# Performance work log

Measured on AMD Instinct MI355X. Metric: run time of the kernel, lower is better.

The kernel has to match this reference:

```python
import jax, jax.numpy as jnp
import numpy as np

STRIDES = (2, 2, 2)  # from init_kwargs


def _sparse_conv3d_transpose(images, kernel, default_value, base_plane, strides):
    """Sparse masked 3D transposed conv driven by a per-pixel depth base plane.

    images:     [B, Hi, Wi, Di, C]  stored slab of active voxels per pixel
    kernel:     [kH, kW, kD, F, C]
    base_plane: [B, Ho, Wo, 1] int  starting VIRTUAL depth of the output slab
    Output virtual depth of voxel (ho, wo, do) is base_plane[ho, wo] + do.
    Input slab start (in input-depth units) at input pixel (hi, wi) is
    base_plane[hi*sH, wi*sW] // sD. SAME-style padding ((k-1)//2).
    Out-of-slab / out-of-bounds taps read default_value (frozen zero).
    """
    B, Hi, Wi, Di, C = images.shape
    k0, k1, k2, F, _ = kernel.shape
    s0, s1, s2 = strides
    bp = base_plane[..., 0]                       # [B, Ho, Wo]
    Ho, Wo = bp.shape[1], bp.shape[2]
    Do = Di * s2
    p0, p1, p2 = (k0 - 1) // 2, (k1 - 1) // 2, (k2 - 1) // 2
    bp_in = bp[:, ::s0, ::s1] // s2               # [B, Hi, Wi] input slab start
    b_idx = jnp.arange(B)[:, None, None]
    vd = bp[..., None] + jnp.arange(Do)           # [B, Ho, Wo, Do] virtual out depth
    ho = jnp.arange(Ho)
    wo = jnp.arange(Wo)
    out = jnp.zeros((B, Ho, Wo, Do, F), images.dtype)
    for kh in range(k0):
        hn = ho + p0 - kh
        hok = (hn % s0 == 0) & (hn >= 0) & (hn < Hi * s0)
        hi = jnp.clip(hn // s0, 0, Hi - 1)
        for kw in range(k1):
            wn = wo + p1 - kw
            wok = (wn % s1 == 0) & (wn >= 0) & (wn < Wi * s1)
            wi = jnp.clip(wn // s1, 0, Wi - 1)
            sp_ok = hok[None, :, None] & wok[None, None, :]              # [1,Ho,Wo]
            bpg = bp_in[b_idx, hi[None, :, None], wi[None, None, :]]     # [B,Ho,Wo]
            for kd in range(k2):
                dn = vd + p2 - kd                                        # [B,Ho,Wo,Do]
                dok = (dn % s2) == 0
                di = dn // s2 - bpg[..., None]
                mask = sp_ok[..., None] & dok & (di >= 0) & (di < Di)
                dic = jnp.clip(di, 0, Di - 1)
                # gather [B,Ho,Wo,Do,C]
                vals = images[b_idx[..., None], hi[None, :, None, None],
                              wi[None, None, :, None], dic]
                vals = jnp.where(mask[..., None], vals, default_value)
                out = out + jnp.einsum('bhwdc,fc->bhwdf', vals, kernel[kh, kw, kd])
    return out


def setup_inputs() -> dict:
    key = jax.random.key(0)
    k1, k2, k3 = jax.random.split(key, 3)
    B, Hi, Wi, Di, C, F = 2, 64, 64, 32, 16, 8
    images = jax.random.normal(k1, (B, Hi, Wi, Di, C), dtype=jnp.float32)
    base_plane = jax.random.randint(k2, (B, Hi * 2, Wi * 2, 1), 0, 16, dtype=jnp.int32)
    kernel = jax.random.normal(k3, (3, 3, 3, F, C), dtype=jnp.float32) * 0.1
    default_value = jnp.zeros((), dtype=jnp.float32)  # frozen, zeros initializer
    return {"images": images, "base_plane": base_plane,
            "kernel": kernel, "default_value": default_value}


def reference(images, base_plane, kernel, default_value):
    return _sparse_conv3d_transpose(images, kernel, default_value, base_plane, STRIDES)
```

## Files before the change

### kernel.cpp

```cpp
#include <hip/hip_runtime.h>

constexpr int Bc  = 2;
constexpr int HiC = 64, WiC = 64, DiC = 32;
constexpr int Cc  = 16, Fc  = 8;
constexpr int HoC = 128, WoC = 128, DoC = 64;
constexpr int IMG_ELEMS = Bc * HiC * WiC * DiC * Cc;

constexpr int SLAB_SHORTS = DiC * Cc;
constexpr int NSLAB       = 18;
constexpr int ZOFF        = NSLAB * SLAB_SHORTS * 2;

typedef __attribute__((ext_vector_type(8))) short short8;
typedef __attribute__((ext_vector_type(4))) float f32x4;

__device__ alignas(16) const float FZERO[8] = {0, 0, 0, 0, 0, 0, 0, 0};

__device__ __forceinline__ unsigned pk2(float x, float y) {
    unsigned ux = __float_as_uint(x), uy = __float_as_uint(y);
    ux += ((ux >> 16) & 1u) + 0x7FFFu;
    uy += ((uy >> 16) & 1u) + 0x7FFFu;
    return (ux >> 16) | (uy & 0xFFFF0000u);
}
__device__ __forceinline__ short8 pack8(float4 a, float4 b) {
    union { unsigned u[4]; short8 s; } r;
    r.u[0] = pk2(a.x, a.y); r.u[1] = pk2(a.z, a.w);
    r.u[2] = pk2(b.x, b.y); r.u[3] = pk2(b.z, b.w);
    return r.s;
}

__device__ __forceinline__ void gload_lds16(const short* g, short* l) {
    __builtin_amdgcn_global_load_lds(
        (const __attribute__((address_space(1))) void*)(unsigned long long)(const void*)g,
        (__attribute__((address_space(3))) void*)(unsigned long long)(void*)l,
        16, 0, 0);
}

__global__ __launch_bounds__(256)
void imgcvt(const float4* __restrict__ in, uint2* __restrict__ outv, int n4) {
    int i = blockIdx.x * 256 + threadIdx.x;
    if (i < n4) {
        float4 v = in[i];
        uint2 o; o.x = pk2(v.x, v.y); o.y = pk2(v.z, v.w);
        outv[i] = o;
    } else if (i < n4 + 8) {
        uint2 z; z.x = 0u; z.y = 0u;
        outv[i] = z;
    }
}

template<int CLS, int CVT>
__device__ __forceinline__ void doCols(const short* __restrict__ slabs,
                                       const float* __restrict__ img32,
                                       const int*   __restrict__ bp,
                                       const float* __restrict__ kern,
                                       float*       __restrict__ out,
                                       float*       __restrict__ ldsw,
                                       int b, int ho, int wo0, int wi0, int lane) {
    constexpr int NP = (CLS == 0) ? 1 : ((CLS == 3) ? 4 : 2);
    constexpr int OP = (NP + 1) / 2;
    constexpr int KH[4][4] = {{1,0,0,0},{1,1,0,0},{0,2,0,0},{0,0,2,2}};
    constexpr int KW[4][4] = {{1,0,0,0},{0,2,0,0},{1,1,0,0},{0,2,0,2}};

    const int quad = lane >> 4, n = lane & 15;
    const int half = quad >> 1, chalf = quad & 1;
    const int chalfB = chalf * 16;

    short8 bE[NP], bO[OP];
    #pragma unroll
    for (int p = 0; p < NP; ++p) {
        const int kp = KH[CLS][p] * 3 + KW[CLS][p];
        const float* wp = (n < Fc)
            ? kern + (kp * 3 + 2 * half) * 128 + n * 16 + chalf * 8 : FZERO;
        bE[p] = pack8(*(const float4*)wp, *(const float4*)(wp + 4));
    }
    #pragma unroll
    for (int pp = 0; pp < OP; ++pp) {
        const int  PA   = (2 * pp < NP) ? 2 * pp : 0;
        const bool hasB = (2 * pp + 1) < NP;
        const int  PB   = hasB ? (2 * pp + 1) : 0;
        const int kpa = KH[CLS][PA] * 3 + KW[CLS][PA];
        const int kpb = KH[CLS][PB] * 3 + KW[CLS][PB];
        const int kp  = half ? kpb : kpa;
        const bool v  = (n < Fc) && (!half || hasB);
        const float* wp = v ? kern + (kp * 3 + 1) * 128 + n * 16 + chalf * 8 : FZERO;
        bO[pp] = pack8(*(const float4*)wp, *(const float4*)(wp + 4));
    }

    int colx[4], bpcol[4], bpgr[4][NP], pxo[4][NP]; bool pvs[4][NP];
    #pragma unroll
    for (int cc = 0; cc < 4; ++cc) {
        const int wo = wo0 + 2 * cc;
        colx[cc]  = __builtin_amdgcn_readfirstlane((b * HoC + ho) * WoC + wo);
        bpcol[cc] = bp[colx[cc]];
        #pragma unroll
        for (int p = 0; p < NP; ++p) {
            const int kh = KH[CLS][p], kw = KW[CLS][p];
            int hi = (ho + 1 - kh) >> 1; hi = hi > HiC - 1 ? HiC - 1 : hi;
            int wi = (wo + 1 - kw) >> 1; wi = wi > WiC - 1 ? WiC - 1 : wi;
            pvs[cc][p] = (kh != 0 || ho + 1 < HoC) && (kw != 0 || wo + 1 < WoC);
            const int sidx =
                __builtin_amdgcn_readfirstlane((b * HoC + 2 * hi) * WoC + 2 * wi);
            bpgr[cc][p] = bp[sidx];
            if constexpr (CVT) {
                pxo[cc][p] = __builtin_amdgcn_readfirstlane(
                                 ((b * HiC + hi) * WiC + wi) * (DiC * Cc));
            } else {
                const int hidx = (kh == 0) ? 1 : 0;
                pxo[cc][p] = __builtin_amdgcn_readfirstlane(
                                 (hidx * 9 + (wi - wi0)) << 10);
            }
        }
    }

    #pragma unroll
    for (int cc = 0; cc < 4; ++cc) {
        const int bp_col = bpcol[cc];
        const int q      = (bp_col + 1) & 1;
        const int baseE  = (bp_col + q + 1) >> 1;
        const int baseO  = (bp_col + 1 - q) >> 1;
        int sE[NP], sO[NP];
        #pragma unroll
        for (int p = 0; p < NP; ++p) {
            const int bpg = bpgr[cc][p] >> 1;
            sE[p] = pvs[cc][p] ? baseE - bpg : -100000;
            sO[p] = pvs[cc][p] ? baseO - bpg : -100000;
        }

        f32x4 accE[2] = {{0.f,0.f,0.f,0.f},{0.f,0.f,0.f,0.f}};
        f32x4 accO[2] = {{0.f,0.f,0.f,0.f},{0.f,0.f,0.f,0.f}};

        #pragma unroll
        for (int g = 0; g < 2; ++g) {
            #pragma unroll
            for (int p = 0; p < NP; ++p) {
                const int  di = sE[p] + 16 * g + n - half;
                const bool ok = (unsigned)di < (unsigned)DiC;
                short8 a;
                if constexpr (CVT) {
                    const float* ap = ok ? img32 + pxo[cc][p] + di * Cc + chalf * 8 : FZERO;
                    a = pack8(*(const float4*)ap, *(const float4*)(ap + 4));
                } else {
                    const int off = ok ? pxo[cc][p] + di * 32 + chalfB : ZOFF;
                    a = *(const short8*)((const char*)slabs + off);
                }
                accE[g] = __builtin_amdgcn_mfma_f32_16x16x32_bf16(a, bE[p], accE[g], 0, 0, 0);
            }
            #pragma unroll
            for (int pp = 0; pp < OP; ++pp) {
                const int  PA   = (2 * pp < NP) ? 2 * pp : 0;
                const bool hasB = (2 * pp + 1) < NP;
                const int  PB   = hasB ? (2 * pp + 1) : 0;
                const int  sOs  = half ? (hasB ? sO[PB] : -100000) : sO[PA];
                const int  pxs  = half ? pxo[cc][PB] : pxo[cc][PA];
                const int  di = sOs + 16 * g + n;
                const bool ok = (unsigned)di < (unsigned)DiC;
                short8 a;
                if constexpr (CVT) {
                    const float* ap = ok ? img32 + pxs + di * Cc + chalf * 8 : FZERO;
                    a = pack8(*(const float4*)ap, *(const float4*)(ap + 4));
                } else {
                    const int off = ok ? pxs + di * 32 + chalfB : ZOFF;
                    a = *(const short8*)((const char*)slabs + off);
                }
                accO[g] = __builtin_amdgcn_mfma_f32_16x16x32_bf16(a, bO[pp], accO[g], 0, 0, 0);
            }
        }

        __builtin_amdgcn_wave_barrier();
        if (n < Fc) {
            #pragma unroll
            for (int g = 0; g < 2; ++g) {
                #pragma unroll
                for (int r = 0; r < 4; ++r) {
                    const int m2 = 16 * g + quad * 4 + r;
                    ldsw[(2 * m2 + q) * Fc + n]     = accE[g][r];
                    ldsw[(2 * m2 + 1 - q) * Fc + n] = accO[g][r];
                }
            }
        }
        __builtin_amdgcn_wave_barrier();
        float* outc = out + (size_t)colx[cc] * (DoC * Fc);
        *(float4*)(outc + lane * 8)     = *(const float4*)(ldsw + lane * 8);
        *(float4*)(outc + lane * 8 + 4) = *(const float4*)(ldsw + lane * 8 + 4);
        __builtin_amdgcn_wave_barrier();
    }
}

template<int CVT>
__global__ __launch_bounds__(256, 3)
void sconv_mfma(const short* __restrict__ img16, const float* __restrict__ img32,
                const int* __restrict__ bp, const float* __restrict__ kern,
                float* __restrict__ out) {
    __shared__ short slabs[NSLAB * SLAB_SHORTS + 8];
    __shared__ float lds[4 * DoC * Fc];
    const int t = threadIdx.x, wv = t >> 6, lane = t & 63;
    const int b = blockIdx.z, ho = blockIdx.y;
    const int wo0 = (blockIdx.x << 4) + (wv & 1) + ((wv >> 1) << 3);
    const int wi0 = blockIdx.x << 3;
    float* ldsw = lds + wv * (DoC * Fc);

    if constexpr (!CVT) {
        const int nSlab = (ho & 1) ? 18 : 9;
        const int hi0 = ho >> 1;
        int hi1 = (ho + 1) >> 1; if (hi1 > HiC - 1) hi1 = HiC - 1;
        for (int s = wv; s < nSlab; s += 4) {
            const int hi = (s >= 9) ? hi1 : hi0;
            int wi = wi0 + ((s >= 9) ? s - 9 : s); if (wi > WiC - 1) wi = WiC - 1;
            const short* g = img16 + (((b * HiC + hi) * WiC + wi) << 9) + lane * 8;
            gload_lds16(g, &slabs[s << 9]);
        }
        if (t < 8) slabs[NSLAB * SLAB_SHORTS + t] = 0;
        __syncthreads();
    }

    if (ho & 1) {
        if (wv & 1) doCols<3, CVT>(slabs, img32, bp, kern, out, ldsw, b, ho, wo0, wi0, lane);
        else        doCols<2, CVT>(slabs, img32, bp, kern, out, ldsw, b, ho, wo0, wi0, lane);
    } else {
        if (wv & 1) doCols<1, CVT>(slabs, img32, bp, kern, out, ldsw, b, ho, wo0, wi0, lane);
        else        doCols<0, CVT>(slabs, img32, bp, kern, out, ldsw, b, ho, wo0, wi0, lane);
    }
}

extern "C" void kernel_launch(void* const* d_in, const int* in_sizes, int n_in,
                              void* d_out, int out_size, void* d_ws, size_t ws_size,
                              hipStream_t stream) {
    const float* images = (const float*)d_in[0];
    const int*   bp     = (const int*)d_in[1];
    const float* kern   = (const float*)d_in[2];
    float* out = (float*)d_out;

    const size_t needWs = ((size_t)IMG_ELEMS + 32) * sizeof(short);

    dim3 grid(WoC / 16, HoC, Bc), block(256);
    if (ws_size >= needWs) {
        const int n4 = IMG_ELEMS / 4;
        hipLaunchKernelGGL(imgcvt, dim3(n4 / 256 + 1), dim3(256), 0, stream,
                           (const float4*)images, (uint2*)d_ws, n4);
        hipLaunchKernelGGL((sconv_mfma<0>), grid, block, 0, stream,
                           (const short*)d_ws, images, bp, kern, out);
    } else {
        hipLaunchKernelGGL((sconv_mfma<1>), grid, block, 0, stream,
                           (const short*)nullptr, images, bp, kern, out);
    }
}
```

Baseline: 98.62 us.

## Fuse fp32-to-bf16 image conversion into slab staging and drop separate convert kernel

Removes the standalone imgcvt kernel and its bf16 workspace copy. Each block now loads fp32 image slabs directly from global memory, packs them to bf16 in registers, and writes them into LDS before the MFMA loop. This saves one kernel launch and a full read/write pass over the image. In exchange, each block reads twice as many bytes per slab, does the packing arithmetic redundantly across the blocks that share slabs, and gives up the async global_load_lds path.

Measured after the change: 97.50 us. No clear change (-1.1%).

```diff
diff --git a/kernel.cpp b/kernel.cpp
--- a/kernel.cpp
+++ b/kernel.cpp
@@ -4,7 +4,6 @@
 constexpr int HiC = 64, WiC = 64, DiC = 32;
 constexpr int Cc  = 16, Fc  = 8;
 constexpr int HoC = 128, WoC = 128, DoC = 64;
-constexpr int IMG_ELEMS = Bc * HiC * WiC * DiC * Cc;
 
 constexpr int SLAB_SHORTS = DiC * Cc;
 constexpr int NSLAB       = 18;
@@ -28,29 +27,8 @@
     return r.s;
 }
 
-__device__ __forceinline__ void gload_lds16(const short* g, short* l) {
-    __builtin_amdgcn_global_load_lds(
-        (const __attribute__((address_space(1))) void*)(unsigned long long)(const void*)g,
-        (__attribute__((address_space(3))) void*)(unsigned long long)(void*)l,
-        16, 0, 0);
-}
-
-__global__ __launch_bounds__(256)
-void imgcvt(const float4* __restrict__ in, uint2* __restrict__ outv, int n4) {
-    int i = blockIdx.x * 256 + threadIdx.x;
-    if (i < n4) {
-        float4 v = in[i];
-        uint2 o; o.x = pk2(v.x, v.y); o.y = pk2(v.z, v.w);
-        outv[i] = o;
-    } else if (i < n4 + 8) {
-        uint2 z; z.x = 0u; z.y = 0u;
-        outv[i] = z;
-    }
-}
-
-template<int CLS, int CVT>
+template<int CLS>
 __device__ __forceinline__ void doCols(const short* __restrict__ slabs,
-                                       const float* __restrict__ img32,
                                        const int*   __restrict__ bp,
                                        const float* __restrict__ kern,
                                        float*       __restrict__ out,
@@ -101,14 +79,9 @@
             const int sidx =
                 __builtin_amdgcn_readfirstlane((b * HoC + 2 * hi) * WoC + 2 * wi);
             bpgr[cc][p] = bp[sidx];
-            if constexpr (CVT) {
-                pxo[cc][p] = __builtin_amdgcn_readfirstlane(
-                                 ((b * HiC + hi) * WiC + wi) * (DiC * Cc));
-            } else {
-                const int hidx = (kh == 0) ? 1 : 0;
-                pxo[cc][p] = __builtin_amdgcn_readfirstlane(
-                                 (hidx * 9 + (wi - wi0)) << 10);
-            }
+            const int hidx = (kh == 0) ? 1 : 0;
+            pxo[cc][p] = __builtin_amdgcn_readfirstlane(
+                             (hidx * 9 + (wi - wi0)) << 10);
         }
     }
 
@@ -135,14 +108,8 @@
             for (int p = 0; p < NP; ++p) {
                 const int  di = sE[p] + 16 * g + n - half;
                 const bool ok = (unsigned)di < (unsigned)DiC;
-                short8 a;
-                if constexpr (CVT) {
-                    const float* ap = ok ? img32 + pxo[cc][p] + di * Cc + chalf * 8 : FZERO;
-                    a = pack8(*(const float4*)ap, *(const float4*)(ap + 4));
-                } else {
-                    const int off = ok ? pxo[cc][p] + di * 32 + chalfB : ZOFF;
-                    a = *(const short8*)((const char*)slabs + off);
-                }
+                const int  off = ok ? pxo[cc][p] + di * 32 + chalfB : ZOFF;
+                short8 a = *(const short8*)((const char*)slabs + off);
                 accE[g] = __builtin_amdgcn_mfma_f32_16x16x32_bf16(a, bE[p], accE[g], 0, 0, 0);
             }
             #pragma unroll
@@ -154,14 +121,8 @@
                 const int  pxs  = half ? pxo[cc][PB] : pxo[cc][PA];
                 const int  di = sOs + 16 * g + n;
                 const bool ok = (unsigned)di < (unsigned)DiC;
-                short8 a;
-                if constexpr (CVT) {
-                    const float* ap = ok ? img32 + pxs + di * Cc + chalf * 8 : FZERO;
-                    a = pack8(*(const float4*)ap, *(const float4*)(ap + 4));
-                } else {
-                    const int off = ok ? pxs + di * 32 + chalfB : ZOFF;
-                    a = *(const short8*)((const char*)slabs + off);
-                }
+                const int  off = ok ? pxs + di * 32 + chalfB : ZOFF;
+                short8 a = *(const short8*)((const char*)slabs + off);
                 accO[g] = __builtin_amdgcn_mfma_f32_16x16x32_bf16(a, bO[pp], accO[g], 0, 0, 0);
             }
         }
@@ -186,11 +147,9 @@
     }
 }
 
-template<int CVT>
 __global__ __launch_bounds__(256, 3)
-void sconv_mfma(const short* __restrict__ img16, const float* __restrict__ img32,
-                const int* __restrict__ bp, const float* __restrict__ kern,
-                float* __restrict__ out) {
+void sconv_mfma(const float* __restrict__ img, const int* __restrict__ bp,
+                const float* __restrict__ kern, float* __restrict__ out) {
     __shared__ short slabs[NSLAB * SLAB_SHORTS + 8];
     __shared__ float lds[4 * DoC * Fc];
     const int t = threadIdx.x, wv = t >> 6, lane = t & 63;
@@ -199,26 +158,30 @@
     const int wi0 = blockIdx.x << 3;
     float* ldsw = lds + wv * (DoC * Fc);
 
-    if constexpr (!CVT) {
-        const int nSlab = (ho & 1) ? 18 : 9;
-        const int hi0 = ho >> 1;
-        int hi1 = (ho + 1) >> 1; if (hi1 > HiC - 1) hi1 = HiC - 1;
-        for (int s = wv; s < nSlab; s += 4) {
+    const int nSlab = (ho & 1) ? 18 : 9;
+    const int hi0 = ho >> 1;
+    int hi1 = (ho + 1) >> 1; if (hi1 > HiC - 1) hi1 = HiC - 1;
+    #pragma unroll
+    for (int k = 0; k < 5; ++k) {
+        const int s = wv + 4 * k;
+        if (s < nSlab) {
             const int hi = (s >= 9) ? hi1 : hi0;
             int wi = wi0 + ((s >= 9) ? s - 9 : s); if (wi > WiC - 1) wi = WiC - 1;
-            const short* g = img16 + (((b * HiC + hi) * WiC + wi) << 9) + lane * 8;
-            gload_lds16(g, &slabs[s << 9]);
-        }
-        if (t < 8) slabs[NSLAB * SLAB_SHORTS + t] = 0;
-        __syncthreads();
-    }
+            const float* g = img + (((b * HiC + hi) * WiC + wi) << 9) + lane * 8;
+            float4 v0 = *(const float4*)g;
+            float4 v1 = *(const float4*)(g + 4);
+            *(short8*)&slabs[(s << 9) + lane * 8] = pack8(v0, v1);
+        }
+    }
+    if (t < 8) slabs[NSLAB * SLAB_SHORTS + t] = 0;
+    __syncthreads();
 
     if (ho & 1) {
-        if (wv & 1) doCols<3, CVT>(slabs, img32, bp, kern, out, ldsw, b, ho, wo0, wi0, lane);
-        else        doCols<2, CVT>(slabs, img32, bp, kern, out, ldsw, b, ho, wo0, wi0, lane);
+        if (wv & 1) doCols<3>(slabs, bp, kern, out, ldsw, b, ho, wo0, wi0, lane);
+        else        doCols<2>(slabs, bp, kern, out, ldsw, b, ho, wo0, wi0, lane);
     } else {
-        if (wv & 1) doCols<1, CVT>(slabs, img32, bp, kern, out, ldsw, b, ho, wo0, wi0, lane);
-        else        doCols<0, CVT>(slabs, img32, bp, kern, out, ldsw, b, ho, wo0, wi0, lane);
+        if (wv & 1) doCols<1>(slabs, bp, kern, out, ldsw, b, ho, wo0, wi0, lane);
+        else        doCols<0>(slabs, bp, kern, out, ldsw, b, ho, wo0, wi0, lane);
     }
 }
 
@@ -229,18 +192,9 @@
     const int*   bp     = (const int*)d_in[1];
     const float* kern   = (const float*)d_in[2];
     float* out = (float*)d_out;
-
-    const size_t needWs = ((size_t)IMG_ELEMS + 32) * sizeof(short);
+    (void)d_ws; (void)ws_size;
 
     dim3 grid(WoC / 16, HoC, Bc), block(256);
-    if (ws_size >= needWs) {
-        const int n4 = IMG_ELEMS / 4;
-        hipLaunchKernelGGL(imgcvt, dim3(n4 / 256 + 1), dim3(256), 0, stream,
-                           (const float4*)images, (uint2*)d_ws, n4);
-        hipLaunchKernelGGL((sconv_mfma<0>), grid, block, 0, stream,
-                           (const short*)d_ws, images, bp, kern, out);
-    } else {
-        hipLaunchKernelGGL((sconv_mfma<1>), grid, block, 0, stream,
-                           (const short*)nullptr, images, bp, kern, out);
-    }
-}
+    hipLaunchKernelGGL(sconv_mfma, grid, block, 0, stream,
+                       images, bp, kern, out);
+}
```
